# Optimization experiments

Measured on AMD Instinct MI355X. Metric: run time of the kernel, lower is better.

Reference implementation:

```python
import jax, jax.numpy as jnp
import numpy as np

B, S, D = 8, 1024, 512
H, Q, V = 8, 64, 64
NEG_INF = -2.0**32 + 1.0  # faithful to the TF module's mask fill value


def setup_inputs() -> dict:
    key = jax.random.key(0)
    ks = jax.random.split(key, 9)
    s = lambda fan_in: 1.0 / np.sqrt(fan_in)
    return {
        "x": jax.random.normal(ks[0], (B, S, D), dtype=jnp.float32),
        "Wq": jax.random.normal(ks[1], (D, Q * H), dtype=jnp.float32) * s(D),
        "bq": jnp.zeros((Q * H,), dtype=jnp.float32),
        "Wk": jax.random.normal(ks[2], (D, Q * H), dtype=jnp.float32) * s(D),
        "bk": jnp.zeros((Q * H,), dtype=jnp.float32),
        "Wv": jax.random.normal(ks[3], (D, V * H), dtype=jnp.float32) * s(D),
        "bv": jnp.zeros((V * H,), dtype=jnp.float32),
        "Wo": jax.random.normal(ks[4], (V * H, D), dtype=jnp.float32) * s(V * H),
        "bo": jnp.zeros((D,), dtype=jnp.float32),
    }


def _split_heads(t, hd):
    # [B,S,h*hd] -> split along last axis into h, concat along axis0 -> [h*B,S,hd]
    b, seq, _ = t.shape
    return t.reshape(b, seq, H, hd).transpose(2, 0, 1, 3).reshape(H * b, seq, hd)


def reference(x, Wq, bq, Wk, bk, Wv, bv, Wo, bo):
    q = _split_heads(x @ Wq + bq, Q)  # [h*B, S, q]
    k = _split_heads(x @ Wk + bk, Q)  # [h*B, S, q]
    v = _split_heads(x @ Wv + bv, V)  # [h*B, S, v]

    score = jnp.einsum("nsq,ntq->nst", q, k)  # [h*B, S, S], NOTE: no 1/sqrt(d) scaling (faithful)
    heatmap_score = score

    # stage == 'train': causal mask, masked entries set to -2^32 + 1
    mask = jnp.tril(jnp.ones((S, S), dtype=bool))
    score = jnp.where(mask, score, jnp.full_like(score, NEG_INF))
    attn = jax.nn.softmax(score, axis=-1)

    wv = jnp.einsum("nst,ntv->nsv", attn, v)  # [h*B, S, v]
    # split along axis0 into h, concat along last axis -> [B, S, h*v]
    wv = wv.reshape(H, B, S, V).transpose(1, 2, 0, 3).reshape(B, S, H * V)
    out = wv @ Wo + bo  # [B, S, D]
    return (out, heatmap_score)
```

## Files before the change

kernel.cpp:

```cpp
#include <hip/hip_runtime.h>


typedef unsigned short u16;
typedef unsigned int u32;
typedef __attribute__((ext_vector_type(8))) short bf8;
typedef __attribute__((ext_vector_type(4))) float f4;

__device__ __forceinline__ u16 f2bf(float f) {
    u32 x = __builtin_bit_cast(u32, f);
    return (u16)((x + 0x7FFFu + ((x >> 16) & 1u)) >> 16);
}

#define MFMA16(a, b, c) __builtin_amdgcn_mfma_f32_16x16x32_bf16((a), (b), (c), 0, 0, 0)

#define GLD16(gp, lp) __builtin_amdgcn_global_load_lds( \
    (const __attribute__((address_space(1))) unsigned int*)(gp), \
    (__attribute__((address_space(3))) unsigned int*)(lp), 16, 0, 0)

__global__ __launch_bounds__(256) void k_cvt_x(const float4* __restrict__ xi,
                                               ushort4* __restrict__ xo)
{
    int idx = blockIdx.x * 256 + threadIdx.x;
    for (int i = idx; i < 1048576; i += 262144) {
        float4 f = xi[i];
        ushort4 o;
        o.x = f2bf(f.x); o.y = f2bf(f.y); o.z = f2bf(f.z); o.w = f2bf(f.w);
        xo[i] = o;
    }
}

__global__ __launch_bounds__(256) void k_cvt_wT(
    const float* __restrict__ Wq, const float* __restrict__ Wk,
    const float* __restrict__ Wv, const float* __restrict__ Wo,
    u16* __restrict__ WqT, u16* __restrict__ WkT,
    u16* __restrict__ WvT, u16* __restrict__ WoT)
{
    const int z = blockIdx.z;
    const float* __restrict__ W = (z == 0) ? Wq : (z == 1) ? Wk : (z == 2) ? Wv : Wo;
    u16* __restrict__ WT        = (z == 0) ? WqT : (z == 1) ? WkT : (z == 2) ? WvT : WoT;

    __shared__ __align__(16) u16 Ts[64 * 72];
    const int k0 = blockIdx.x * 64, c0 = blockIdx.y * 64;
    const int tid = threadIdx.x;
    const int r = tid >> 4, cc = (tid & 15) * 4;
    #pragma unroll
    for (int rr = r; rr < 64; rr += 16) {
        float4 f = *(const float4*)&W[(size_t)(k0 + rr) * 512 + c0 + cc];
        Ts[(cc + 0) * 72 + rr] = f2bf(f.x);
        Ts[(cc + 1) * 72 + rr] = f2bf(f.y);
        Ts[(cc + 2) * 72 + rr] = f2bf(f.z);
        Ts[(cc + 3) * 72 + rr] = f2bf(f.w);
    }
    __syncthreads();
    #pragma unroll
    for (int i = 0; i < 2; ++i) {
        int gi = tid + i * 256;
        int cr = gi >> 3, g = gi & 7;
        bf8 v = *(bf8*)&Ts[cr * 72 + g * 8];
        *(bf8*)&WT[(size_t)(c0 + cr) * 512 + k0 + g * 8] = v;
    }
}

__global__ __launch_bounds__(256) void k_qkv(
    const u16* __restrict__ xb,
    const u16* __restrict__ WqT, const u16* __restrict__ WkT, const u16* __restrict__ WvT,
    const float* __restrict__ bq, const float* __restrict__ bk, const float* __restrict__ bv,
    u16* __restrict__ qb, u16* __restrict__ kb, u16* __restrict__ vT)
{
    const int which = blockIdx.z;
    const u16* __restrict__ WT     = (which == 0) ? WqT : (which == 1) ? WkT : WvT;
    const float* __restrict__ bias = (which == 0) ? bq : (which == 1) ? bk : bv;

    const int colTile = blockIdx.x * 128;
    const int rowTile = blockIdx.y * 128;

    __shared__ __align__(16) u16 As[128 * 64];
    __shared__ __align__(16) u16 Bs[128 * 64];

    const int tid = threadIdx.x;
    const int lane = tid & 63, w = tid >> 6;
    const int lm = lane & 15, kq = lane >> 4;
    const int mB = (w >> 1) * 64, nB = (w & 1) * 64;

    const int sr = lane >> 3;
    const int sg = (lane & 7) ^ sr;

    f4 acc[4][4] = {};

    for (int k0 = 0; k0 < 512; k0 += 64) {
        __syncthreads();
        #pragma unroll
        for (int i = 0; i < 4; ++i) {
            const int rb = w * 32 + i * 8;
            GLD16(&xb[(size_t)(rowTile + rb + sr) * 512 + k0 + sg * 8], &As[rb * 64]);
            GLD16(&WT[(size_t)(colTile + rb + sr) * 512 + k0 + sg * 8], &Bs[rb * 64]);
        }
        __syncthreads();
        #pragma unroll
        for (int ks = 0; ks < 2; ++ks) {
            bf8 a[4], b[4];
            #pragma unroll
            for (int mi = 0; mi < 4; ++mi)
                a[mi] = *(bf8*)&As[(mB + mi * 16 + lm) * 64 + (((ks * 4 + kq) ^ (lm & 7)) * 8)];
            #pragma unroll
            for (int ni = 0; ni < 4; ++ni)
                b[ni] = *(bf8*)&Bs[(nB + ni * 16 + lm) * 64 + (((ks * 4 + kq) ^ (lm & 7)) * 8)];
            #pragma unroll
            for (int mi = 0; mi < 4; ++mi)
                #pragma unroll
                for (int ni = 0; ni < 4; ++ni)
                    acc[mi][ni] = MFMA16(a[mi], b[ni], acc[mi][ni]);
        }
    }

    if (which < 2) {
        u16* __restrict__ outp = (which == 0) ? qb : kb;
        #pragma unroll
        for (int mi = 0; mi < 4; ++mi) {
            const int r0 = rowTile + mB + mi * 16 + kq * 4;
            #pragma unroll
            for (int ni = 0; ni < 4; ++ni) {
                const int c = colTile + nB + ni * 16 + lm;
                const float bv_ = bias[c];
                const int h = c >> 6, hd = c & 63;
                #pragma unroll
                for (int rg = 0; rg < 4; ++rg) {
                    const int rr = r0 + rg;
                    const int b = rr >> 10, s = rr & 1023;
                    outp[(size_t)(((h * 8 + b) << 10) + s) * 64 + hd] = f2bf(acc[mi][ni][rg] + bv_);
                }
            }
        }
    } else {
        #pragma unroll
        for (int mi = 0; mi < 4; ++mi) {
            const int r0 = rowTile + mB + mi * 16 + kq * 4;
            const int b = r0 >> 10, s0 = r0 & 1023;
            #pragma unroll
            for (int ni = 0; ni < 4; ++ni) {
                const int c = colTile + nB + ni * 16 + lm;
                const float bv_ = bias[c];
                const int h = c >> 6, hd = c & 63;
                ushort4 pk;
                pk.x = f2bf(acc[mi][ni][0] + bv_);
                pk.y = f2bf(acc[mi][ni][1] + bv_);
                pk.z = f2bf(acc[mi][ni][2] + bv_);
                pk.w = f2bf(acc[mi][ni][3] + bv_);
                *(ushort4*)&vT[(size_t)((h * 8 + b) * 64 + hd) * 1024 + s0] = pk;
            }
        }
    }
}

__global__ __launch_bounds__(256) void k_attn(
    const u16* __restrict__ qb, const u16* __restrict__ kb, const u16* __restrict__ vT,
    float* __restrict__ heat, u16* __restrict__ wvb)
{
    const int bid = blockIdx.x;
    const int sT = (bid < 256) ? (7 - (bid >> 6)) : ((bid >> 6) - 4);
    const int n = bid & 63;
    const int s0 = sT * 128;

    __shared__ __align__(16) u16 KPs[128 * 136];
    __shared__ __align__(16) u16 Vs[64 * 128];

    const int tid = threadIdx.x;
    const int lane = tid & 63, w = tid >> 6;
    const int lm = lane & 15, kq = lane >> 4;
    const int mB = w * 32;

    const int sr = lane >> 3, sg = (lane & 7) ^ sr;
    const int vr = lane >> 4, vg = lane & 15;

    const u16* __restrict__ qn = qb + (size_t)n * 65536;
    const u16* __restrict__ kn = kb + (size_t)n * 65536;
    const u16* __restrict__ vn = vT + (size_t)n * 65536;
    float* __restrict__ hp = heat + ((size_t)n << 20);

    bf8 aq[2][2];
    #pragma unroll
    for (int mi = 0; mi < 2; ++mi)
        #pragma unroll
        for (int ks = 0; ks < 2; ++ks)
            aq[mi][ks] = *(const bf8*)&qn[(size_t)(s0 + mB + mi * 16 + lm) * 64 + ks * 32 + kq * 8];

    f4 accO[2][4] = {};
    float m_i[2][4], l_i[2][4];
    #pragma unroll
    for (int mi = 0; mi < 2; ++mi)
        #pragma unroll
        for (int rg = 0; rg < 4; ++rg) { m_i[mi][rg] = -3.0e38f; l_i[mi][rg] = 0.f; }

    for (int tt = 0; tt < 8; ++tt) {
        const int t0 = tt * 128;
        const bool causal = (tt <= sT);

        __syncthreads();
        #pragma unroll
        for (int i = 0; i < 4; ++i) {
            const int rb = w * 32 + i * 8;
            GLD16(&kn[(size_t)(t0 + rb + sr) * 64 + sg * 8], &KPs[rb * 64]);
        }
        if (causal) {
            #pragma unroll
            for (int i = 0; i < 4; ++i) {
                const int rb = w * 16 + i * 4;
                const int r = rb + vr;
                GLD16(&vn[(size_t)r * 1024 + t0 + ((vg ^ (r & 7)) * 8)], &Vs[rb * 128]);
            }
        }
        __syncthreads();

        f4 accS[2][8] = {};
        #pragma unroll
        for (int ks = 0; ks < 2; ++ks) {
            bf8 b[8];
            #pragma unroll
            for (int ni = 0; ni < 8; ++ni)
                b[ni] = *(bf8*)&KPs[(ni * 16 + lm) * 64 + (((ks * 4 + kq) ^ (lm & 7)) * 8)];
            #pragma unroll
            for (int mi = 0; mi < 2; ++mi)
                #pragma unroll
                for (int ni = 0; ni < 8; ++ni)
                    accS[mi][ni] = MFMA16(aq[mi][ks], b[ni], accS[mi][ni]);
        }

        #pragma unroll
        for (int mi = 0; mi < 2; ++mi) {
            #pragma unroll
            for (int rg = 0; rg < 4; ++rg) {
                float* rowp = &hp[(size_t)(s0 + mB + mi * 16 + kq * 4 + rg) * 1024 + t0 + lm];
                #pragma unroll
                for (int ni = 0; ni < 8; ++ni) rowp[ni * 16] = accS[mi][ni][rg];
            }
        }

        if (causal) {
            __syncthreads();
            const bool diag = (tt == sT);
            #pragma unroll
            for (int mi = 0; mi < 2; ++mi) {
                #pragma unroll
                for (int rg = 0; rg < 4; ++rg) {
                    const int srow = s0 + mB + mi * 16 + kq * 4 + rg;
                    float tm = -3.0e38f;
                    #pragma unroll
                    for (int ni = 0; ni < 8; ++ni) {
                        float sv = accS[mi][ni][rg];
                        if (diag && (t0 + ni * 16 + lm > srow)) sv = -3.0e38f;
                        tm = fmaxf(tm, sv);
                    }
                    tm = fmaxf(tm, __shfl_xor(tm, 1));
                    tm = fmaxf(tm, __shfl_xor(tm, 2));
                    tm = fmaxf(tm, __shfl_xor(tm, 4));
                    tm = fmaxf(tm, __shfl_xor(tm, 8));
                    const float mn = fmaxf(m_i[mi][rg], tm);
                    const float alpha = __expf(m_i[mi][rg] - mn);
                    float rs = 0.f;
                    #pragma unroll
                    for (int ni = 0; ni < 8; ++ni) {
                        float sv = accS[mi][ni][rg];
                        const bool ok = !diag || (t0 + ni * 16 + lm <= srow);
                        float p = ok ? __expf(sv - mn) : 0.f;
                        rs += p;
                        KPs[(mB + mi * 16 + kq * 4 + rg) * 136 + ni * 16 + lm] = f2bf(p);
                    }
                    rs += __shfl_xor(rs, 1);
                    rs += __shfl_xor(rs, 2);
                    rs += __shfl_xor(rs, 4);
                    rs += __shfl_xor(rs, 8);
                    l_i[mi][rg] = l_i[mi][rg] * alpha + rs;
                    m_i[mi][rg] = mn;
                    #pragma unroll
                    for (int vni = 0; vni < 4; ++vni) accO[mi][vni][rg] *= alpha;
                }
            }

            #pragma unroll
            for (int ks = 0; ks < 4; ++ks) {
                bf8 a[2], b[4];
                #pragma unroll
                for (int mi = 0; mi < 2; ++mi)
                    a[mi] = *(bf8*)&KPs[(mB + mi * 16 + lm) * 136 + ks * 32 + kq * 8];
                #pragma unroll
                for (int vni = 0; vni < 4; ++vni)
                    b[vni] = *(bf8*)&Vs[(vni * 16 + lm) * 128 + (((ks * 4 + kq) ^ (lm & 7)) * 8)];
                #pragma unroll
                for (int mi = 0; mi < 2; ++mi)
                    #pragma unroll
                    for (int vni = 0; vni < 4; ++vni)
                        accO[mi][vni] = MFMA16(a[mi], b[vni], accO[mi][vni]);
            }
        }
    }

    u16* __restrict__ wn = wvb + (size_t)n * 65536;
    #pragma unroll
    for (int mi = 0; mi < 2; ++mi) {
        #pragma unroll
        for (int rg = 0; rg < 4; ++rg) {
            const float li = 1.0f / l_i[mi][rg];
            const int s = s0 + mB + mi * 16 + kq * 4 + rg;
            #pragma unroll
            for (int vni = 0; vni < 4; ++vni)
                wn[(size_t)s * 64 + vni * 16 + lm] = f2bf(accO[mi][vni][rg] * li);
        }
    }
}

__global__ __launch_bounds__(256) void k_out(
    const u16* __restrict__ wvb, const u16* __restrict__ WoT, const float* __restrict__ bo,
    float* __restrict__ outp)
{
    const int colTile = blockIdx.x * 128;
    const int rowTile = blockIdx.y * 128;
    const int b = rowTile >> 10, s0 = rowTile & 1023;

    __shared__ __align__(16) u16 As[128 * 64];
    __shared__ __align__(16) u16 Bs[128 * 64];

    const int tid = threadIdx.x;
    const int lane = tid & 63, w = tid >> 6;
    const int lm = lane & 15, kq = lane >> 4;
    const int mB = (w >> 1) * 64, nB = (w & 1) * 64;

    const int sr = lane >> 3;
    const int sg = (lane & 7) ^ sr;

    f4 acc[4][4] = {};

    for (int k0 = 0; k0 < 512; k0 += 64) {
        const int h = k0 >> 6;
        const u16* __restrict__ abase = wvb + (size_t)((h * 8 + b) * 1024 + s0) * 64;
        __syncthreads();
        #pragma unroll
        for (int i = 0; i < 4; ++i) {
            const int rb = w * 32 + i * 8;
            GLD16(&abase[(size_t)(rb + sr) * 64 + sg * 8], &As[rb * 64]);
            GLD16(&WoT[(size_t)(colTile + rb + sr) * 512 + k0 + sg * 8], &Bs[rb * 64]);
        }
        __syncthreads();
        #pragma unroll
        for (int ks = 0; ks < 2; ++ks) {
            bf8 a[4], b2[4];
            #pragma unroll
            for (int mi = 0; mi < 4; ++mi)
                a[mi] = *(bf8*)&As[(mB + mi * 16 + lm) * 64 + (((ks * 4 + kq) ^ (lm & 7)) * 8)];
            #pragma unroll
            for (int ni = 0; ni < 4; ++ni)
                b2[ni] = *(bf8*)&Bs[(nB + ni * 16 + lm) * 64 + (((ks * 4 + kq) ^ (lm & 7)) * 8)];
            #pragma unroll
            for (int mi = 0; mi < 4; ++mi)
                #pragma unroll
                for (int ni = 0; ni < 4; ++ni)
                    acc[mi][ni] = MFMA16(a[mi], b2[ni], acc[mi][ni]);
        }
    }

    #pragma unroll
    for (int mi = 0; mi < 4; ++mi) {
        const int r0 = rowTile + mB + mi * 16 + kq * 4;
        #pragma unroll
        for (int ni = 0; ni < 4; ++ni) {
            const int c = colTile + nB + ni * 16 + lm;
            const float bv_ = bo[c];
            #pragma unroll
            for (int rg = 0; rg < 4; ++rg)
                outp[(size_t)(r0 + rg) * 512 + c] = acc[mi][ni][rg] + bv_;
        }
    }
}

extern "C" void kernel_launch(void* const* d_in, const int* in_sizes, int n_in,
                              void* d_out, int out_size, void* d_ws, size_t ws_size,
                              hipStream_t stream)
{
    (void)in_sizes; (void)n_in; (void)out_size; (void)ws_size;

    const float* x  = (const float*)d_in[0];
    const float* Wq = (const float*)d_in[1];
    const float* bq = (const float*)d_in[2];
    const float* Wk = (const float*)d_in[3];
    const float* bk = (const float*)d_in[4];
    const float* Wv = (const float*)d_in[5];
    const float* bv = (const float*)d_in[6];
    const float* Wo = (const float*)d_in[7];
    const float* bo = (const float*)d_in[8];

    float* outp = (float*)d_out;
    float* heat = outp + 4194304;

    u16* ws16 = (u16*)d_ws;
    u16* xb  = ws16;
    u16* WqT = xb  + 4194304;
    u16* WkT = WqT + 262144;
    u16* WvT = WkT + 262144;
    u16* WoT = WvT + 262144;
    u16* qb  = WoT + 262144;
    u16* kb  = qb  + 4194304;
    u16* vT  = kb  + 4194304;
    u16* wvb = vT  + 4194304;

    k_cvt_x <<<1024, 256, 0, stream>>>((const float4*)x, (ushort4*)xb);
    k_cvt_wT<<<dim3(8, 8, 4), 256, 0, stream>>>(Wq, Wk, Wv, Wo, WqT, WkT, WvT, WoT);
    k_qkv   <<<dim3(4, 64, 3), 256, 0, stream>>>(xb, WqT, WkT, WvT, bq, bk, bv, qb, kb, vT);
    k_attn  <<<dim3(512), 256, 0, stream>>>(qb, kb, vT, heat, wvb);
    k_out   <<<dim3(4, 64), 256, 0, stream>>>(wvb, WoT, bo, outp);
}
```

Measured before the change: 392.0 us.

## Double-buffer K/V tiles in attention and reuse the K buffer for P

```diff
diff --git a/kernel.cpp b/kernel.cpp
--- a/kernel.cpp
+++ b/kernel.cpp
@@ -161,8 +161,8 @@
     const int n = bid & 63;
     const int s0 = sT * 128;
 
-    __shared__ __align__(16) u16 KPs[128 * 136];
-    __shared__ __align__(16) u16 Vs[64 * 128];
+    __shared__ __align__(16) u16 Kb[2][128 * 64];
+    __shared__ __align__(16) u16 Vb[2][64 * 128];
 
     const int tid = threadIdx.x;
     const int lane = tid & 63, w = tid >> 6;
@@ -177,6 +177,18 @@
     const u16* __restrict__ vn = vT + (size_t)n * 65536;
     float* __restrict__ hp = heat + ((size_t)n << 20);
 
+    #pragma unroll
+    for (int i = 0; i < 4; ++i) {
+        const int rb = w * 32 + i * 8;
+        GLD16(&kn[(size_t)(rb + sr) * 64 + sg * 8], &Kb[0][rb * 64]);
+    }
+    #pragma unroll
+    for (int i = 0; i < 4; ++i) {
+        const int rb = w * 16 + i * 4;
+        const int r = rb + vr;
+        GLD16(&vn[(size_t)r * 1024 + ((vg ^ (r & 7)) * 8)], &Vb[0][rb * 128]);
+    }
+
     bf8 aq[2][2];
     #pragma unroll
     for (int mi = 0; mi < 2; ++mi)
@@ -191,39 +203,48 @@
         #pragma unroll
         for (int rg = 0; rg < 4; ++rg) { m_i[mi][rg] = -3.0e38f; l_i[mi][rg] = 0.f; }
 
-    for (int tt = 0; tt < 8; ++tt) {
+    int c = 0;
+    for (int tt = 0; tt < 8; ++tt, c ^= 1) {
         const int t0 = tt * 128;
         const bool causal = (tt <= sT);
+        u16* __restrict__ Kc = &Kb[c][0];
+        u16* __restrict__ Vc = &Vb[c][0];
 
         __syncthreads();
-        #pragma unroll
-        for (int i = 0; i < 4; ++i) {
-            const int rb = w * 32 + i * 8;
-            GLD16(&kn[(size_t)(t0 + rb + sr) * 64 + sg * 8], &KPs[rb * 64]);
-        }
-        if (causal) {
+
+        if (tt < 7) {
+            u16* __restrict__ Kn2 = &Kb[c ^ 1][0];
             #pragma unroll
             for (int i = 0; i < 4; ++i) {
-                const int rb = w * 16 + i * 4;
-                const int r = rb + vr;
-                GLD16(&vn[(size_t)r * 1024 + t0 + ((vg ^ (r & 7)) * 8)], &Vs[rb * 128]);
-            }
-        }
-        __syncthreads();
+                const int rb = w * 32 + i * 8;
+                GLD16(&kn[(size_t)(t0 + 128 + rb + sr) * 64 + sg * 8], &Kn2[rb * 64]);
+            }
+            if (tt + 1 <= sT) {
+                u16* __restrict__ Vn2 = &Vb[c ^ 1][0];
+                #pragma unroll
+                for (int i = 0; i < 4; ++i) {
+                    const int rb = w * 16 + i * 4;
+                    const int r = rb + vr;
+                    GLD16(&vn[(size_t)r * 1024 + t0 + 128 + ((vg ^ (r & 7)) * 8)], &Vn2[rb * 128]);
+                }
+            }
+        }
 
         f4 accS[2][8] = {};
+        __builtin_amdgcn_s_setprio(1);
         #pragma unroll
         for (int ks = 0; ks < 2; ++ks) {
             bf8 b[8];
             #pragma unroll
             for (int ni = 0; ni < 8; ++ni)
-                b[ni] = *(bf8*)&KPs[(ni * 16 + lm) * 64 + (((ks * 4 + kq) ^ (lm & 7)) * 8)];
+                b[ni] = *(bf8*)&Kc[(ni * 16 + lm) * 64 + (((ks * 4 + kq) ^ (lm & 7)) * 8)];
             #pragma unroll
             for (int mi = 0; mi < 2; ++mi)
                 #pragma unroll
                 for (int ni = 0; ni < 8; ++ni)
                     accS[mi][ni] = MFMA16(aq[mi][ks], b[ni], accS[mi][ni]);
         }
+        __builtin_amdgcn_s_setprio(0);
 
         #pragma unroll
         for (int mi = 0; mi < 2; ++mi) {
@@ -231,12 +252,16 @@
             for (int rg = 0; rg < 4; ++rg) {
                 float* rowp = &hp[(size_t)(s0 + mB + mi * 16 + kq * 4 + rg) * 1024 + t0 + lm];
                 #pragma unroll
-                for (int ni = 0; ni < 8; ++ni) rowp[ni * 16] = accS[mi][ni][rg];
+                for (int ni = 0; ni < 8; ++ni)
+                    __builtin_nontemporal_store(accS[mi][ni][rg], &rowp[ni * 16]);
             }
         }
 
         if (causal) {
-            __syncthreads();
+            asm volatile("s_waitcnt lgkmcnt(0)" ::: "memory");
+            __builtin_amdgcn_s_barrier();
+            __builtin_amdgcn_sched_barrier(0);
+
             const bool diag = (tt == sT);
             #pragma unroll
             for (int mi = 0; mi < 2; ++mi) {
@@ -263,7 +288,7 @@
                         const bool ok = !diag || (t0 + ni * 16 + lm <= srow);
                         float p = ok ? __expf(sv - mn) : 0.f;
                         rs += p;
-                        KPs[(mB + mi * 16 + kq * 4 + rg) * 136 + ni * 16 + lm] = f2bf(p);
+                        accS[mi][ni][rg] = p;
                     }
                     rs += __shfl_xor(rs, 1);
                     rs += __shfl_xor(rs, 2);
@@ -277,19 +302,45 @@
             }
 
             #pragma unroll
-            for (int ks = 0; ks < 4; ++ks) {
-                bf8 a[2], b[4];
-                #pragma unroll
-                for (int mi = 0; mi < 2; ++mi)
-                    a[mi] = *(bf8*)&KPs[(mB + mi * 16 + lm) * 136 + ks * 32 + kq * 8];
-                #pragma unroll
-                for (int vni = 0; vni < 4; ++vni)
-                    b[vni] = *(bf8*)&Vs[(vni * 16 + lm) * 128 + (((ks * 4 + kq) ^ (lm & 7)) * 8)];
-                #pragma unroll
-                for (int mi = 0; mi < 2; ++mi)
+            for (int half = 0; half < 2; ++half) {
+                #pragma unroll
+                for (int mi = 0; mi < 2; ++mi) {
+                    #pragma unroll
+                    for (int rg = 0; rg < 4; ++rg) {
+                        const int prow = mB + mi * 16 + kq * 4 + rg;
+                        #pragma unroll
+                        for (int nl = 0; nl < 4; ++nl) {
+                            const float p = accS[mi][half * 4 + nl][rg];
+                            Kc[prow * 64 + (((nl * 2 + (lm >> 3)) ^ (prow & 7)) * 8) + (lm & 7)] = f2bf(p);
+                        }
+                    }
+                }
+                asm volatile("s_waitcnt lgkmcnt(0)" ::: "memory");
+                __builtin_amdgcn_sched_barrier(0);
+
+                __builtin_amdgcn_s_setprio(1);
+                #pragma unroll
+                for (int kl = 0; kl < 2; ++kl) {
+                    const int ks = half * 2 + kl;
+                    bf8 a[2], b[4];
+                    #pragma unroll
+                    for (int mi = 0; mi < 2; ++mi)
+                        a[mi] = *(bf8*)&Kc[(mB + mi * 16 + lm) * 64 + (((kl * 4 + kq) ^ (lm & 7)) * 8)];
                     #pragma unroll
                     for (int vni = 0; vni < 4; ++vni)
-                        accO[mi][vni] = MFMA16(a[mi], b[vni], accO[mi][vni]);
+                        b[vni] = *(bf8*)&Vc[(vni * 16 + lm) * 128 + (((ks * 4 + kq) ^ (lm & 7)) * 8)];
+                    #pragma unroll
+                    for (int mi = 0; mi < 2; ++mi)
+                        #pragma unroll
+                        for (int vni = 0; vni < 4; ++vni)
+                            accO[mi][vni] = MFMA16(a[mi], b[vni], accO[mi][vni]);
+                }
+                __builtin_amdgcn_s_setprio(0);
+
+                if (half == 0) {
+                    asm volatile("s_waitcnt lgkmcnt(0)" ::: "memory");
+                    __builtin_amdgcn_sched_barrier(0);
+                }
             }
         }
     }
@@ -366,7 +417,8 @@
             const float bv_ = bo[c];
             #pragma unroll
             for (int rg = 0; rg < 4; ++rg)
-                outp[(size_t)(r0 + rg) * 512 + c] = acc[mi][ni][rg] + bv_;
+                __builtin_nontemporal_store(acc[mi][ni][rg] + bv_,
+                                            &outp[(size_t)(r0 + rg) * 512 + c]);
         }
     }
 }
```

New measurement: 389.1 us. About the same (-0.7%).
